# Kernel optimization log

Measured on AMD Instinct MI355X. Metric: run time of the kernel, lower is better.

Reference implementation:

```python
import jax, jax.numpy as jnp
import numpy as np

MERGE_K = 3   # merge_kernel
DS_K = 3      # ds_kernel (avg-pool kernel)
STRIDE = 2


def _unfold(x, kernel, stride):
    """Torch-style F.pad + unfold(2).unfold(3): x [N,C,H,W] -> [N,Ho,Wo,K,C],
    K = kernel**2 in row-major (dh, dw) order, padding = kernel//2 with zeros."""
    pad = kernel // 2
    N, C, H, W = x.shape
    Ho, Wo = H // stride, W // stride
    xp = jnp.pad(x, ((0, 0), (0, 0), (pad, pad), (pad, pad)))
    pats = [
        xp[:, :, di:di + stride * (Ho - 1) + 1:stride,
               dj:dj + stride * (Wo - 1) + 1:stride]
        for di in range(kernel) for dj in range(kernel)
    ]
    p = jnp.stack(pats, axis=-1)          # [N,C,Ho,Wo,K]
    return p.transpose(0, 2, 3, 4, 1)     # [N,Ho,Wo,K,C]


def setup_inputs() -> dict:
    key = jax.random.key(0)
    x = jax.random.normal(key, (32, 768, 56, 56), dtype=jnp.float32)
    return {"x": x}


def reference(x):
    # compute_kq=False: k = q = x
    # AvgPool2d(3, stride=2, padding=1), count_include_pad=True -> mean over
    # zero-padded 3x3 windows == mean over K axis of the unfold.
    q = _unfold(x, DS_K, STRIDE).mean(axis=3)   # [N,Ho,Wo,C]
    kv = _unfold(x, MERGE_K, STRIDE)            # [N,Ho,Wo,K,C]; k and v are identical unfolds of x
    scores = jnp.einsum('nhwc,nhwkc->nhwk', q, kv) / MERGE_K  # divide by merge_kernel (=3), per source
    attn = jax.nn.softmax(scores, axis=-1)      # [N,Ho,Wo,K]
    y = jnp.einsum('nhwk,nhwkc->nhwc', attn, kv)  # weighted merge
    return y.transpose(0, 3, 1, 2)              # [N,C,Ho,Wo]
```

## Files before the change

### kernel.cpp

```cpp
#include <hip/hip_runtime.h>


constexpr int N_  = 32;
constexpr int C_  = 768;
constexpr int H_  = 56;
constexpr int W_  = 56;
constexpr int HO_ = 28;
constexpr int WO_ = 28;
constexpr int NPIX = N_ * HO_ * WO_;

constexpr int K1_CB     = 16;
constexpr int K1_NCHUNK = C_ / K1_CB;
constexpr int K1_TW     = 58;
constexpr int K1_TILE   = K1_CB * 3 * K1_TW;

__global__ __launch_bounds__(256)
void scores_kernel(const float* __restrict__ x, float* __restrict__ scores) {
    __shared__ float tile_raw[4 + K1_TILE];
    __shared__ float sred[8 * WO_ * 9];
    float* tile = tile_raw + 4;

    const int tid   = threadIdx.x;
    const int blk   = blockIdx.x;
    const int chunk = blk / (N_ * HO_);
    const int nho   = blk % (N_ * HO_);
    const int n     = nho / HO_;
    const int ho    = nho % HO_;
    const int cbase = chunk * K1_CB;
    const int row0  = 2 * ho - 1;

    for (int i = tid; i < 4 + K1_TILE; i += 256) tile_raw[i] = 0.f;
    __syncthreads();

    const float* xb = x + (size_t)n * (C_ * H_ * W_);
    for (int i = tid; i < 672; i += 256) {
        int c   = i / 42;
        int rem = i - c * 42;
        int r   = rem / 14;
        int kk  = rem - r * 14;
        int grow = row0 + r;
        if (grow >= 0) {
            float4 v = *(const float4*)(xb + ((size_t)(cbase + c) * H_ + grow) * W_ + 4 * kk);
            float* d = &tile[c * (3 * K1_TW) + r * K1_TW + 4 * kk];
            d[0] = v.x; d[1] = v.y; d[2] = v.z; d[3] = v.w;
        }
    }
    __syncthreads();

    const int wo = tid % WO_;
    const int g  = tid / WO_;
    if (g < 8) {
        float sacc[9];
#pragma unroll
        for (int k = 0; k < 9; ++k) sacc[k] = 0.f;
#pragma unroll
        for (int cc = 0; cc < 2; ++cc) {
            const float* tp = &tile[(g * 2 + cc) * (3 * K1_TW) + 2 * wo - 1];
            float w0 = tp[0],          w1 = tp[1],            w2 = tp[2];
            float w3 = tp[K1_TW],      w4 = tp[K1_TW + 1],    w5 = tp[K1_TW + 2];
            float w6 = tp[2 * K1_TW],  w7 = tp[2 * K1_TW + 1], w8 = tp[2 * K1_TW + 2];
            float q = (w0 + w1 + w2 + w3 + w4 + w5 + w6 + w7 + w8) * (1.f / 9.f);
            sacc[0] += q * w0; sacc[1] += q * w1; sacc[2] += q * w2;
            sacc[3] += q * w3; sacc[4] += q * w4; sacc[5] += q * w5;
            sacc[6] += q * w6; sacc[7] += q * w7; sacc[8] += q * w8;
        }
#pragma unroll
        for (int k = 0; k < 9; ++k) sred[(g * WO_ + wo) * 9 + k] = sacc[k];
    }
    __syncthreads();

    if (tid < WO_ * 9) {
        int wo2 = tid / 9, k = tid - wo2 * 9;
        float t = 0.f;
#pragma unroll
        for (int g2 = 0; g2 < 8; ++g2) t += sred[(g2 * WO_ + wo2) * 9 + k];
        atomicAdd(&scores[((size_t)nho * WO_ + wo2) * 9 + k], t * (1.f / 3.f));
    }
}

__global__ __launch_bounds__(256)
void softmax_kernel(float* __restrict__ scores) {
    int p = blockIdx.x * 256 + threadIdx.x;
    if (p >= NPIX) return;
    float* s = scores + (size_t)p * 9;
    float v[9];
#pragma unroll
    for (int k = 0; k < 9; ++k) v[k] = s[k];
    float m = v[0];
#pragma unroll
    for (int k = 1; k < 9; ++k) m = fmaxf(m, v[k]);
    float d = 0.f;
#pragma unroll
    for (int k = 0; k < 9; ++k) { v[k] = __expf(v[k] - m); d += v[k]; }
    float inv = 1.f / d;
#pragma unroll
    for (int k = 0; k < 9; ++k) s[k] = v[k] * inv;
}

constexpr int K3_TW = 58;

__global__ __launch_bounds__(256)
void merge_kernel(const float* __restrict__ x, const float* __restrict__ attn,
                  float* __restrict__ out) {
    __shared__ float tile_raw[4 + K3_TW * K3_TW];
    float* tile = tile_raw + 4;

    const int tid = threadIdx.x;
    const int blk = blockIdx.x;
    const int n   = blk / C_;
    const int c   = blk - n * C_;

    for (int i = tid; i < 4 + K3_TW * K3_TW; i += 256) tile_raw[i] = 0.f;
    __syncthreads();

    const float* xp = x + ((size_t)n * C_ + c) * (H_ * W_);
    for (int i = tid; i < 784; i += 256) {
        int r  = i / 14;
        int kk = i - r * 14;
        float4 v = *(const float4*)(xp + (size_t)r * W_ + 4 * kk);
        float* d = &tile[(r + 1) * K3_TW + 4 * kk];
        d[0] = v.x; d[1] = v.y; d[2] = v.z; d[3] = v.w;
    }
    __syncthreads();

    float* op = out + ((size_t)n * C_ + c) * (HO_ * WO_);
    const float* ap = attn + (size_t)n * (HO_ * WO_) * 9;
    for (int p = tid; p < HO_ * WO_; p += 256) {
        int ho = p / WO_, wo = p - ho * WO_;
        const float* a  = &ap[(size_t)p * 9];
        const float* tp = &tile[(size_t)(2 * ho) * K3_TW + 2 * wo - 1];
        float y = a[0] * tp[0]           + a[1] * tp[1]            + a[2] * tp[2]
                + a[3] * tp[K3_TW]       + a[4] * tp[K3_TW + 1]    + a[5] * tp[K3_TW + 2]
                + a[6] * tp[2 * K3_TW]   + a[7] * tp[2 * K3_TW + 1] + a[8] * tp[2 * K3_TW + 2];
        op[p] = y;
    }
}

extern "C" void kernel_launch(void* const* d_in, const int* in_sizes, int n_in,
                              void* d_out, int out_size, void* d_ws, size_t ws_size,
                              hipStream_t stream) {
    const float* x   = (const float*)d_in[0];
    float* out       = (float*)d_out;
    float* scores    = (float*)d_ws;

    hipMemsetAsync(d_ws, 0, (size_t)NPIX * 9 * sizeof(float), stream);
    scores_kernel<<<dim3(K1_NCHUNK * N_ * HO_), dim3(256), 0, stream>>>(x, scores);
    softmax_kernel<<<dim3((NPIX + 255) / 256), dim3(256), 0, stream>>>(scores);
    merge_kernel<<<dim3(N_ * C_), dim3(256), 0, stream>>>(x, scores, out);
}
```

Measured before the change: 520.5 us.

## Restructure scores kernel to loop over channel subchunks with far fewer atomics

The scores kernel now has each block handle two output rows and 192 channels, streaming 16-channel sub-tiles through shared memory with in-register accumulation. This replaces 48 chunks of 16 channels each and cuts the atomicAdd traffic and block count. It also folds the 1/9 pooling scale into the final 1/27 factor. The softmax kernel stages its scores through shared memory for coalesced float4 access, and the merge kernel caches the per-image attention weights in shared memory. In exchange there is more shared memory per block, a serial loop inside each block, and fewer blocks to hide latency.

```diff
diff --git a/kernel.cpp b/kernel.cpp
--- a/kernel.cpp
+++ b/kernel.cpp
@@ -9,81 +9,102 @@
 constexpr int WO_ = 28;
 constexpr int NPIX = N_ * HO_ * WO_;
 
-constexpr int K1_CB     = 16;
-constexpr int K1_NCHUNK = C_ / K1_CB;
+constexpr int K1_CHUNKS = 4;
+constexpr int K1_CCH    = C_ / K1_CHUNKS;
+constexpr int K1_SC     = 16;
+constexpr int K1_NSUB   = K1_CCH / K1_SC;
 constexpr int K1_TW     = 58;
-constexpr int K1_TILE   = K1_CB * 3 * K1_TW;
+constexpr int K1_TR     = 5;
 
 __global__ __launch_bounds__(256)
 void scores_kernel(const float* __restrict__ x, float* __restrict__ scores) {
-    __shared__ float tile_raw[4 + K1_TILE];
-    __shared__ float sred[8 * WO_ * 9];
-    float* tile = tile_raw + 4;
+    __shared__ float tile[K1_SC * K1_TR * K1_TW];
+    __shared__ float sred[4 * 56 * 9];
 
     const int tid   = threadIdx.x;
     const int blk   = blockIdx.x;
-    const int chunk = blk / (N_ * HO_);
-    const int nho   = blk % (N_ * HO_);
-    const int n     = nho / HO_;
-    const int ho    = nho % HO_;
-    const int cbase = chunk * K1_CB;
-    const int row0  = 2 * ho - 1;
+    const int chunk = blk / (N_ * 14);
+    const int rem   = blk - chunk * (N_ * 14);
+    const int n     = rem / 14;
+    const int ho2   = rem - n * 14;
+    const int c0    = chunk * K1_CCH;
+    const int row0  = 4 * ho2 - 1;
 
-    for (int i = tid; i < 4 + K1_TILE; i += 256) tile_raw[i] = 0.f;
-    __syncthreads();
+    for (int i = tid; i < K1_SC * K1_TR * K1_TW; i += 256) tile[i] = 0.f;
 
-    const float* xb = x + (size_t)n * (C_ * H_ * W_);
-    for (int i = tid; i < 672; i += 256) {
-        int c   = i / 42;
-        int rem = i - c * 42;
-        int r   = rem / 14;
-        int kk  = rem - r * 14;
-        int grow = row0 + r;
-        if (grow >= 0) {
-            float4 v = *(const float4*)(xb + ((size_t)(cbase + c) * H_ + grow) * W_ + 4 * kk);
-            float* d = &tile[c * (3 * K1_TW) + r * K1_TW + 4 * kk];
-            d[0] = v.x; d[1] = v.y; d[2] = v.z; d[3] = v.w;
+    const int g  = tid >> 6;
+    const int p  = tid & 63;
+    const int hr = p >> 5;
+    const int wo = p & 31;
+    const bool act = wo < WO_;
+
+    float acc[9];
+#pragma unroll
+    for (int k = 0; k < 9; ++k) acc[k] = 0.f;
+
+    const float* xb = x + ((size_t)n * C_ + c0) * (H_ * W_);
+
+    for (int sub = 0; sub < K1_NSUB; ++sub) {
+        __syncthreads();
+        for (int i = tid; i < K1_SC * K1_TR * 14; i += 256) {
+            int c    = i / (K1_TR * 14);
+            int r2   = i - c * (K1_TR * 14);
+            int r    = r2 / 14;
+            int kk   = r2 - r * 14;
+            int grow = row0 + r;
+            if (grow >= 0) {
+                float4 v = *(const float4*)(xb + ((size_t)(sub * K1_SC + c) * H_ + grow) * W_ + 4 * kk);
+                float* d = &tile[(c * K1_TR + r) * K1_TW + 1 + 4 * kk];
+                d[0] = v.x; d[1] = v.y; d[2] = v.z; d[3] = v.w;
+            }
+        }
+        __syncthreads();
+        if (act) {
+#pragma unroll
+            for (int cc = 0; cc < K1_SC / 4; ++cc) {
+                const int c = cc * 4 + g;
+                const float* tp = &tile[(c * K1_TR + 2 * hr) * K1_TW + 2 * wo];
+                float2 r0 = *(const float2*)(tp);
+                float  w2 = tp[2];
+                float2 r1 = *(const float2*)(tp + K1_TW);
+                float  w5 = tp[K1_TW + 2];
+                float2 r2 = *(const float2*)(tp + 2 * K1_TW);
+                float  w8 = tp[2 * K1_TW + 2];
+                float w0 = r0.x, w1 = r0.y, w3 = r1.x, w4 = r1.y, w6 = r2.x, w7 = r2.y;
+                float q = ((w0 + w1) + (w2 + w3)) + ((w4 + w5) + (w6 + w7)) + w8;
+                acc[0] += q * w0; acc[1] += q * w1; acc[2] += q * w2;
+                acc[3] += q * w3; acc[4] += q * w4; acc[5] += q * w5;
+                acc[6] += q * w6; acc[7] += q * w7; acc[8] += q * w8;
+            }
         }
     }
-    __syncthreads();
 
-    const int wo = tid % WO_;
-    const int g  = tid / WO_;
-    if (g < 8) {
-        float sacc[9];
+    if (act) {
+        const int s = hr * 28 + wo;
 #pragma unroll
-        for (int k = 0; k < 9; ++k) sacc[k] = 0.f;
-#pragma unroll
-        for (int cc = 0; cc < 2; ++cc) {
-            const float* tp = &tile[(g * 2 + cc) * (3 * K1_TW) + 2 * wo - 1];
-            float w0 = tp[0],          w1 = tp[1],            w2 = tp[2];
-            float w3 = tp[K1_TW],      w4 = tp[K1_TW + 1],    w5 = tp[K1_TW + 2];
-            float w6 = tp[2 * K1_TW],  w7 = tp[2 * K1_TW + 1], w8 = tp[2 * K1_TW + 2];
-            float q = (w0 + w1 + w2 + w3 + w4 + w5 + w6 + w7 + w8) * (1.f / 9.f);
-            sacc[0] += q * w0; sacc[1] += q * w1; sacc[2] += q * w2;
-            sacc[3] += q * w3; sacc[4] += q * w4; sacc[5] += q * w5;
-            sacc[6] += q * w6; sacc[7] += q * w7; sacc[8] += q * w8;
-        }
-#pragma unroll
-        for (int k = 0; k < 9; ++k) sred[(g * WO_ + wo) * 9 + k] = sacc[k];
+        for (int k = 0; k < 9; ++k) sred[(g * 56 + s) * 9 + k] = acc[k];
     }
     __syncthreads();
-
-    if (tid < WO_ * 9) {
-        int wo2 = tid / 9, k = tid - wo2 * 9;
-        float t = 0.f;
-#pragma unroll
-        for (int g2 = 0; g2 < 8; ++g2) t += sred[(g2 * WO_ + wo2) * 9 + k];
-        atomicAdd(&scores[((size_t)nho * WO_ + wo2) * 9 + k], t * (1.f / 3.f));
+    for (int i = tid; i < 56 * 9; i += 256) {
+        int s = i / 9, k = i - s * 9;
+        float t = sred[s * 9 + k]         + sred[(56 + s) * 9 + k]
+                + sred[(112 + s) * 9 + k] + sred[(168 + s) * 9 + k];
+        int hrr = s / 28, woo = s - hrr * 28;
+        int ho  = 2 * ho2 + hrr;
+        atomicAdd(&scores[(((size_t)n * HO_ + ho) * WO_ + woo) * 9 + k], t * (1.f / 27.f));
     }
 }
 
 __global__ __launch_bounds__(256)
 void softmax_kernel(float* __restrict__ scores) {
-    int p = blockIdx.x * 256 + threadIdx.x;
-    if (p >= NPIX) return;
-    float* s = scores + (size_t)p * 9;
+    __shared__ float sbuf[256 * 9];
+    const int tid = threadIdx.x;
+    float4* gb = (float4*)(scores + (size_t)blockIdx.x * (256 * 9));
+    float4* lb = (float4*)sbuf;
+    for (int i = tid; i < 576; i += 256) lb[i] = gb[i];
+    __syncthreads();
     float v[9];
+    float* s = sbuf + tid * 9;
 #pragma unroll
     for (int k = 0; k < 9; ++k) v[k] = s[k];
     float m = v[0];
@@ -95,6 +116,8 @@
     float inv = 1.f / d;
 #pragma unroll
     for (int k = 0; k < 9; ++k) s[k] = v[k] * inv;
+    __syncthreads();
+    for (int i = tid; i < 576; i += 256) gb[i] = lb[i];
 }
 
 constexpr int K3_TW = 58;
@@ -103,6 +126,7 @@
 void merge_kernel(const float* __restrict__ x, const float* __restrict__ attn,
                   float* __restrict__ out) {
     __shared__ float tile_raw[4 + K3_TW * K3_TW];
+    __shared__ float attn_s[HO_ * WO_ * 9];
     float* tile = tile_raw + 4;
 
     const int tid = threadIdx.x;
@@ -121,16 +145,18 @@
         float* d = &tile[(r + 1) * K3_TW + 4 * kk];
         d[0] = v.x; d[1] = v.y; d[2] = v.z; d[3] = v.w;
     }
+    const float4* ag = (const float4*)(attn + (size_t)n * (HO_ * WO_ * 9));
+    float4* as = (float4*)attn_s;
+    for (int i = tid; i < (HO_ * WO_ * 9) / 4; i += 256) as[i] = ag[i];
     __syncthreads();
 
     float* op = out + ((size_t)n * C_ + c) * (HO_ * WO_);
-    const float* ap = attn + (size_t)n * (HO_ * WO_) * 9;
     for (int p = tid; p < HO_ * WO_; p += 256) {
         int ho = p / WO_, wo = p - ho * WO_;
-        const float* a  = &ap[(size_t)p * 9];
+        const float* a  = &attn_s[p * 9];
         const float* tp = &tile[(size_t)(2 * ho) * K3_TW + 2 * wo - 1];
-        float y = a[0] * tp[0]           + a[1] * tp[1]            + a[2] * tp[2]
-                + a[3] * tp[K3_TW]       + a[4] * tp[K3_TW + 1]    + a[5] * tp[K3_TW + 2]
+        float y = a[0] * tp[0]           + a[1] * tp[1]             + a[2] * tp[2]
+                + a[3] * tp[K3_TW]       + a[4] * tp[K3_TW + 1]     + a[5] * tp[K3_TW + 2]
                 + a[6] * tp[2 * K3_TW]   + a[7] * tp[2 * K3_TW + 1] + a[8] * tp[2 * K3_TW + 2];
         op[p] = y;
     }
@@ -144,7 +170,7 @@
     float* scores    = (float*)d_ws;
 
     hipMemsetAsync(d_ws, 0, (size_t)NPIX * 9 * sizeof(float), stream);
-    scores_kernel<<<dim3(K1_NCHUNK * N_ * HO_), dim3(256), 0, stream>>>(x, scores);
-    softmax_kernel<<<dim3((NPIX + 255) / 256), dim3(256), 0, stream>>>(scores);
+    scores_kernel<<<dim3(K1_CHUNKS * N_ * 14), dim3(256), 0, stream>>>(x, scores);
+    softmax_kernel<<<dim3(NPIX / 256), dim3(256), 0, stream>>>(scores);
     merge_kernel<<<dim3(N_ * C_), dim3(256), 0, stream>>>(x, scores, out);
 }
```

Result: slower. 624.3 us (+19.9%).

## Fuse scores, softmax and merge into one per-row kernel with double-buffered staging

Applied to the files above, without the earlier changes.

Replaces the memset plus scores, softmax and merge kernels with a single kernel where each block handles one output row of one image. The block loops over channel chunks twice, first accumulating scores in registers and then computing the weighted merge, using double-buffered shared-memory tiles. This removes the atomics, the global scores round trip, and extra launches. In exchange it reduces the grid to far fewer blocks, serializes many chunk loads per block, and may lower memory-level parallelism.

```diff
diff --git a/kernel.cpp b/kernel.cpp
--- a/kernel.cpp
+++ b/kernel.cpp
@@ -7,144 +7,130 @@
 constexpr int W_  = 56;
 constexpr int HO_ = 28;
 constexpr int WO_ = 28;
-constexpr int NPIX = N_ * HO_ * WO_;
 
-constexpr int K1_CB     = 16;
-constexpr int K1_NCHUNK = C_ / K1_CB;
-constexpr int K1_TW     = 58;
-constexpr int K1_TILE   = K1_CB * 3 * K1_TW;
+constexpr int SC   = 16;
+constexpr int NSUB = C_ / SC;
+constexpr int TW   = 58;
+constexpr int TILE = SC * 3 * TW;
+constexpr int HW_  = H_ * W_;
 
 __global__ __launch_bounds__(256)
-void scores_kernel(const float* __restrict__ x, float* __restrict__ scores) {
-    __shared__ float tile_raw[4 + K1_TILE];
-    __shared__ float sred[8 * WO_ * 9];
-    float* tile = tile_raw + 4;
+void fused_kernel(const float* __restrict__ x, float* __restrict__ out) {
+    __shared__ float raw[4 + TILE + 4 + TILE];
+    __shared__ float sred[8 * 252];
+    __shared__ float attn_s[252];
+    float* bufA = raw + 4;
+    float* bufB = raw + 4 + TILE + 4;
 
-    const int tid   = threadIdx.x;
-    const int blk   = blockIdx.x;
-    const int chunk = blk / (N_ * HO_);
-    const int nho   = blk % (N_ * HO_);
-    const int n     = nho / HO_;
-    const int ho    = nho % HO_;
-    const int cbase = chunk * K1_CB;
-    const int row0  = 2 * ho - 1;
+    const int tid  = threadIdx.x;
+    const int blk  = blockIdx.x;
+    const int n    = blk / HO_;
+    const int ho   = blk - n * HO_;
+    const int row0 = 2 * ho - 1;
 
-    for (int i = tid; i < 4 + K1_TILE; i += 256) tile_raw[i] = 0.f;
+    for (int i = tid; i < 2 * TILE + 8; i += 256) raw[i] = 0.f;
+
+    const float* xb = x + (size_t)n * C_ * HW_;
+
+    auto stage = [&](float* tb, int sub) {
+        const float* xs = xb + (size_t)(sub * SC) * HW_;
+        for (int i = tid; i < SC * 3 * 14; i += 256) {
+            int c    = i / 42;
+            int rem  = i - c * 42;
+            int r    = rem / 14;
+            int kk   = rem - r * 14;
+            int grow = row0 + r;
+            if (grow >= 0) {
+                float4 v = *(const float4*)(xs + (size_t)c * HW_ + (size_t)grow * W_ + 4 * kk);
+                float* d = &tb[(c * 3 + r) * TW + 4 * kk];
+                d[0] = v.x; d[1] = v.y; d[2] = v.z; d[3] = v.w;
+            }
+        }
+    };
+
+    const int g   = tid >> 5;
+    const int wo  = tid & 31;
+    const bool act = wo < WO_;
+
+    float acc[9];
+#pragma unroll
+    for (int k = 0; k < 9; ++k) acc[k] = 0.f;
+
+    stage(bufA, 0);
     __syncthreads();
+    for (int sub = 0; sub < NSUB; ++sub) {
+        float* cur = (sub & 1) ? bufB : bufA;
+        float* nxt = (sub & 1) ? bufA : bufB;
+        if (sub + 1 < NSUB) stage(nxt, sub + 1);
+        if (act) {
+#pragma unroll
+            for (int cc = 0; cc < 2; ++cc) {
+                const float* tp = &cur[((g * 2 + cc) * 3) * TW + 2 * wo - 1];
+                float w0 = tp[0],        w1 = tp[1],          w2 = tp[2];
+                float w3 = tp[TW],       w4 = tp[TW + 1],     w5 = tp[TW + 2];
+                float w6 = tp[2 * TW],   w7 = tp[2 * TW + 1], w8 = tp[2 * TW + 2];
+                float q = ((w0 + w1) + (w2 + w3)) + ((w4 + w5) + (w6 + w7)) + w8;
+                acc[0] += q * w0; acc[1] += q * w1; acc[2] += q * w2;
+                acc[3] += q * w3; acc[4] += q * w4; acc[5] += q * w5;
+                acc[6] += q * w6; acc[7] += q * w7; acc[8] += q * w8;
+            }
+        }
+        __syncthreads();
+    }
 
-    const float* xb = x + (size_t)n * (C_ * H_ * W_);
-    for (int i = tid; i < 672; i += 256) {
-        int c   = i / 42;
-        int rem = i - c * 42;
-        int r   = rem / 14;
-        int kk  = rem - r * 14;
-        int grow = row0 + r;
-        if (grow >= 0) {
-            float4 v = *(const float4*)(xb + ((size_t)(cbase + c) * H_ + grow) * W_ + 4 * kk);
-            float* d = &tile[c * (3 * K1_TW) + r * K1_TW + 4 * kk];
-            d[0] = v.x; d[1] = v.y; d[2] = v.z; d[3] = v.w;
-        }
+    if (act) {
+#pragma unroll
+        for (int k = 0; k < 9; ++k) sred[g * 252 + wo * 9 + k] = acc[k];
+    }
+    __syncthreads();
+    stage(bufA, 0);
+    if (tid < 252) {
+        float t = 0.f;
+#pragma unroll
+        for (int g2 = 0; g2 < 8; ++g2) t += sred[g2 * 252 + tid];
+        attn_s[tid] = t * (1.f / 27.f);
+    }
+    __syncthreads();
+    if (tid < WO_) {
+        float* s = &attn_s[tid * 9];
+        float v[9];
+#pragma unroll
+        for (int k = 0; k < 9; ++k) v[k] = s[k];
+        float m = v[0];
+#pragma unroll
+        for (int k = 1; k < 9; ++k) m = fmaxf(m, v[k]);
+        float d = 0.f;
+#pragma unroll
+        for (int k = 0; k < 9; ++k) { v[k] = __expf(v[k] - m); d += v[k]; }
+        float inv = 1.f / d;
+#pragma unroll
+        for (int k = 0; k < 9; ++k) s[k] = v[k] * inv;
     }
     __syncthreads();
 
-    const int wo = tid % WO_;
-    const int g  = tid / WO_;
-    if (g < 8) {
-        float sacc[9];
-#pragma unroll
-        for (int k = 0; k < 9; ++k) sacc[k] = 0.f;
-#pragma unroll
-        for (int cc = 0; cc < 2; ++cc) {
-            const float* tp = &tile[(g * 2 + cc) * (3 * K1_TW) + 2 * wo - 1];
-            float w0 = tp[0],          w1 = tp[1],            w2 = tp[2];
-            float w3 = tp[K1_TW],      w4 = tp[K1_TW + 1],    w5 = tp[K1_TW + 2];
-            float w6 = tp[2 * K1_TW],  w7 = tp[2 * K1_TW + 1], w8 = tp[2 * K1_TW + 2];
-            float q = (w0 + w1 + w2 + w3 + w4 + w5 + w6 + w7 + w8) * (1.f / 9.f);
-            sacc[0] += q * w0; sacc[1] += q * w1; sacc[2] += q * w2;
-            sacc[3] += q * w3; sacc[4] += q * w4; sacc[5] += q * w5;
-            sacc[6] += q * w6; sacc[7] += q * w7; sacc[8] += q * w8;
+    float* op = out + (size_t)n * C_ * (HO_ * WO_) + (size_t)ho * WO_;
+    for (int sub = 0; sub < NSUB; ++sub) {
+        float* cur = (sub & 1) ? bufB : bufA;
+        float* nxt = (sub & 1) ? bufA : bufB;
+        if (sub + 1 < NSUB) stage(nxt, sub + 1);
+        for (int i = tid; i < SC * WO_; i += 256) {
+            int c = i / WO_;
+            int w = i - c * WO_;
+            const float* a  = &attn_s[w * 9];
+            const float* tp = &cur[(c * 3) * TW + 2 * w - 1];
+            float y = a[0] * tp[0]        + a[1] * tp[1]          + a[2] * tp[2]
+                    + a[3] * tp[TW]       + a[4] * tp[TW + 1]     + a[5] * tp[TW + 2]
+                    + a[6] * tp[2 * TW]   + a[7] * tp[2 * TW + 1] + a[8] * tp[2 * TW + 2];
+            op[(size_t)(sub * SC + c) * (HO_ * WO_) + w] = y;
         }
-#pragma unroll
-        for (int k = 0; k < 9; ++k) sred[(g * WO_ + wo) * 9 + k] = sacc[k];
-    }
-    __syncthreads();
-
-    if (tid < WO_ * 9) {
-        int wo2 = tid / 9, k = tid - wo2 * 9;
-        float t = 0.f;
-#pragma unroll
-        for (int g2 = 0; g2 < 8; ++g2) t += sred[(g2 * WO_ + wo2) * 9 + k];
-        atomicAdd(&scores[((size_t)nho * WO_ + wo2) * 9 + k], t * (1.f / 3.f));
-    }
-}
-
-__global__ __launch_bounds__(256)
-void softmax_kernel(float* __restrict__ scores) {
-    int p = blockIdx.x * 256 + threadIdx.x;
-    if (p >= NPIX) return;
-    float* s = scores + (size_t)p * 9;
-    float v[9];
-#pragma unroll
-    for (int k = 0; k < 9; ++k) v[k] = s[k];
-    float m = v[0];
-#pragma unroll
-    for (int k = 1; k < 9; ++k) m = fmaxf(m, v[k]);
-    float d = 0.f;
-#pragma unroll
-    for (int k = 0; k < 9; ++k) { v[k] = __expf(v[k] - m); d += v[k]; }
-    float inv = 1.f / d;
-#pragma unroll
-    for (int k = 0; k < 9; ++k) s[k] = v[k] * inv;
-}
-
-constexpr int K3_TW = 58;
-
-__global__ __launch_bounds__(256)
-void merge_kernel(const float* __restrict__ x, const float* __restrict__ attn,
-                  float* __restrict__ out) {
-    __shared__ float tile_raw[4 + K3_TW * K3_TW];
-    float* tile = tile_raw + 4;
-
-    const int tid = threadIdx.x;
-    const int blk = blockIdx.x;
-    const int n   = blk / C_;
-    const int c   = blk - n * C_;
-
-    for (int i = tid; i < 4 + K3_TW * K3_TW; i += 256) tile_raw[i] = 0.f;
-    __syncthreads();
-
-    const float* xp = x + ((size_t)n * C_ + c) * (H_ * W_);
-    for (int i = tid; i < 784; i += 256) {
-        int r  = i / 14;
-        int kk = i - r * 14;
-        float4 v = *(const float4*)(xp + (size_t)r * W_ + 4 * kk);
-        float* d = &tile[(r + 1) * K3_TW + 4 * kk];
-        d[0] = v.x; d[1] = v.y; d[2] = v.z; d[3] = v.w;
-    }
-    __syncthreads();
-
-    float* op = out + ((size_t)n * C_ + c) * (HO_ * WO_);
-    const float* ap = attn + (size_t)n * (HO_ * WO_) * 9;
-    for (int p = tid; p < HO_ * WO_; p += 256) {
-        int ho = p / WO_, wo = p - ho * WO_;
-        const float* a  = &ap[(size_t)p * 9];
-        const float* tp = &tile[(size_t)(2 * ho) * K3_TW + 2 * wo - 1];
-        float y = a[0] * tp[0]           + a[1] * tp[1]            + a[2] * tp[2]
-                + a[3] * tp[K3_TW]       + a[4] * tp[K3_TW + 1]    + a[5] * tp[K3_TW + 2]
-                + a[6] * tp[2 * K3_TW]   + a[7] * tp[2 * K3_TW + 1] + a[8] * tp[2 * K3_TW + 2];
-        op[p] = y;
+        __syncthreads();
     }
 }
 
 extern "C" void kernel_launch(void* const* d_in, const int* in_sizes, int n_in,
                               void* d_out, int out_size, void* d_ws, size_t ws_size,
                               hipStream_t stream) {
-    const float* x   = (const float*)d_in[0];
-    float* out       = (float*)d_out;
-    float* scores    = (float*)d_ws;
-
-    hipMemsetAsync(d_ws, 0, (size_t)NPIX * 9 * sizeof(float), stream);
-    scores_kernel<<<dim3(K1_NCHUNK * N_ * HO_), dim3(256), 0, stream>>>(x, scores);
-    softmax_kernel<<<dim3((NPIX + 255) / 256), dim3(256), 0, stream>>>(scores);
-    merge_kernel<<<dim3(N_ * C_), dim3(256), 0, stream>>>(x, scores, out);
+    const float* x = (const float*)d_in[0];
+    float* out     = (float*)d_out;
+    fused_kernel<<<dim3(N_ * HO_), dim3(256), 0, stream>>>(x, out);
 }
```

New measurement: 599.4 us. +15.2%, slower.
